# Kernel optimization log

Measured on AMD Instinct MI355X. Metric: run time of the kernel, lower is better.

Reference implementation:

```python
import jax, jax.numpy as jnp
import numpy as np

EPS = 1e-6
LAMB = 0.1
ITERS = 3


def setup_inputs() -> dict:
    key = jax.random.key(0)
    k = jax.random.split(key, 6)
    bi, bt, R, W, D = 128, 128, 36, 50, 1024
    return {
        "img_cls": jax.random.normal(k[0], (bi, D), jnp.float32),
        "imgs": jax.random.normal(k[1], (bi, R, D), jnp.float32),
        "cap_cls": jax.random.normal(k[2], (bt, D), jnp.float32),
        "caps": jax.random.normal(k[3], (bt, W, D), jnp.float32),
        "img_lens": jax.random.randint(k[4], (bi,), 1, R + 1, jnp.int32),
        "cap_lens": jax.random.randint(k[5], (bt,), 1, W + 1, jnp.int32),
    }


def _bregman(cost, mask, r, c):
    # P = exp(-cost/lamb) (masked entries have cost=+inf -> P=0), then
    # iterative row/col rescaling toward marginals r, c.
    P = jnp.where(mask, jnp.exp(-cost / LAMB), 0.0)
    P = P / (jnp.sum(P, axis=(-2, -1), keepdims=True) + EPS)
    for _ in range(ITERS):
        u = P.sum(axis=-1) + EPS          # [bi,bt,R]
        P = P * (r / u)[..., None]
        v = P.sum(axis=-2) + EPS          # [bi,bt,W]
        P = P * (c / v)[:, :, None, :]
    return P


def reference(img_cls, imgs, cap_cls, caps, img_lens, cap_lens):
    imgs = imgs + EPS
    caps = caps + EPS
    # prepend cls token
    imgs = jnp.concatenate([img_cls[:, None, :], imgs], axis=1)   # [bi,R+1,D]
    caps = jnp.concatenate([cap_cls[:, None, :], caps], axis=1)   # [bt,W+1,D]
    imgs = imgs / jnp.linalg.norm(imgs, axis=-1, keepdims=True)
    caps = caps / jnp.linalg.norm(caps, axis=-1, keepdims=True)
    # fine-grained cosine sims: [bi, bt, R+1, W+1]
    fg_sims = jnp.einsum("ird,twd->itrw", imgs, caps)
    il = img_lens + 1
    cl = cap_lens + 1
    R1, W1 = imgs.shape[1], caps.shape[1]
    rmask = jnp.arange(R1)[None, :] < il[:, None]   # [bi,R+1]
    wmask = jnp.arange(W1)[None, :] < cl[:, None]   # [bt,W+1]
    mask = rmask[:, None, :, None] & wmask[None, :, None, :]  # [bi,bt,R+1,W+1]
    # _ave_init: uniform marginals over valid rows/cols
    rvalid = mask.any(axis=-1).astype(fg_sims.dtype)  # [bi,bt,R+1]
    cvalid = mask.any(axis=-2).astype(fg_sims.dtype)  # [bi,bt,W+1]
    r = rvalid / rvalid.sum(axis=-1, keepdims=True)
    c = cvalid / cvalid.sum(axis=-1, keepdims=True)
    cost = 1.0 - fg_sims
    tp = _bregman(cost, mask, r, c)
    sims = jnp.sum(fg_sims * tp * mask.astype(fg_sims.dtype), axis=(-2, -1))
    return sims  # [bi, bt]
```

## Files before the change

### kernel.cpp

```cpp
#include <hip/hip_runtime.h>
#include <hip/hip_fp16.h>

#define EPSF 1e-6f

typedef _Float16 f16x8 __attribute__((ext_vector_type(8)));
typedef float f32x4 __attribute__((ext_vector_type(4)));

#define BK 64
#define SMEM_BYTES 37888
#define BUF_BYTES 10240

#define AS1 __attribute__((address_space(1)))
#define AS3 __attribute__((address_space(3)))

#define VM_WAIT(N) asm volatile("s_waitcnt vmcnt(" #N ")" ::: "memory")
#define LGKM0()    asm volatile("s_waitcnt lgkmcnt(0)" ::: "memory")

__device__ __forceinline__ float wave_sum_fast(float x) {
    asm volatile(
        "s_nop 1\n\t"
        "v_add_f32 %0, %0, %0 quad_perm:[1,0,3,2] row_mask:0xf bank_mask:0xf bound_ctrl:0\n\t"
        "s_nop 1\n\t"
        "v_add_f32 %0, %0, %0 quad_perm:[2,3,0,1] row_mask:0xf bank_mask:0xf bound_ctrl:0\n\t"
        "s_nop 1\n\t"
        "v_add_f32 %0, %0, %0 row_half_mirror row_mask:0xf bank_mask:0xf bound_ctrl:0\n\t"
        "s_nop 1\n\t"
        "v_add_f32 %0, %0, %0 row_mirror row_mask:0xf bank_mask:0xf bound_ctrl:0\n\t"
        "s_nop 1\n\t"
        "v_add_f32 %0, %0, %0 row_bcast:15 row_mask:0xf bank_mask:0xf bound_ctrl:0\n\t"
        "s_nop 1\n\t"
        "v_add_f32 %0, %0, %0 row_bcast:31 row_mask:0xf bank_mask:0xf bound_ctrl:0"
        : "+v"(x));
    return __int_as_float(__builtin_amdgcn_readlane(__float_as_int(x), 63));
}

__global__ __launch_bounds__(256) void norm_kernel(
        const float* __restrict__ img_cls, const float* __restrict__ imgs,
        const float* __restrict__ cap_cls, const float* __restrict__ caps,
        __half* __restrict__ Ah, __half* __restrict__ Bh) {
    __shared__ float red[4];
    const int row = blockIdx.x;
    const int tid = threadIdx.x;

    const float* src = nullptr;
    __half* dsth;
    float eps_add = EPSF;
    if (row < 64 * 80) {
        const int g = row / 80, r = row % 80;
        dsth = Ah + (size_t)row * 1024 + tid * 4;
        int i = -1, rr = 0;
        if (r < 37)      { i = 2 * g;     rr = r; }
        else if (r < 74) { i = 2 * g + 1; rr = r - 37; }
        if (i >= 0) {
            if (rr == 0) { src = img_cls + (size_t)i * 1024; eps_add = 0.0f; }
            else         { src = imgs + ((size_t)i * 36 + (rr - 1)) * 1024; }
        }
    } else {
        const int row2 = row - 64 * 80;
        const int t = row2 >> 6, r = row2 & 63;
        const int n = r >> 4, fr = r & 15;
        const int kt = tid >> 3, q4 = (tid >> 1) & 3, j = (tid & 1) * 4;
        dsth = Bh + ((size_t)(t * 32 + kt) * 4 + n) * 512 + (q4 * 16 + fr) * 8 + j;
        if (r == 0)       { src = cap_cls + (size_t)t * 1024; eps_add = 0.0f; }
        else if (r <= 50) { src = caps + ((size_t)t * 50 + (r - 1)) * 1024; }
    }

    if (src == nullptr) {
        ushort4 z; z.x = z.y = z.z = z.w = 0;
        *reinterpret_cast<ushort4*>(dsth) = z;
        return;
    }

    float4 v = reinterpret_cast<const float4*>(src)[tid];
    v.x += eps_add; v.y += eps_add; v.z += eps_add; v.w += eps_add;
    float ss = v.x * v.x + v.y * v.y + v.z * v.z + v.w * v.w;
    #pragma unroll
    for (int m = 1; m <= 32; m <<= 1) ss += __shfl_xor(ss, m);
    if ((tid & 63) == 0) red[tid >> 6] = ss;
    __syncthreads();
    const float tot = red[0] + red[1] + red[2] + red[3];
    const float rn = 1.0f / sqrtf(tot);

    ushort4 o;
    o.x = __half_as_ushort(__float2half(v.x * rn));
    o.y = __half_as_ushort(__float2half(v.y * rn));
    o.z = __half_as_ushort(__float2half(v.z * rn));
    o.w = __half_as_ushort(__float2half(v.w * rn));
    *reinterpret_cast<ushort4*>(dsth) = o;
}

__device__ __forceinline__ void stage_octA(const __half* __restrict__ Ag,
                                           __half* buf, int kb, int o, size_t lofs) {
    const __half* src = Ag + (size_t)o * 8192 + kb + lofs;
    __builtin_amdgcn_global_load_lds((const AS1 void*)src,
                                     (AS3 void*)(buf + o * 512), 16, 0, 0);
}

__device__ __forceinline__ void stage_A(const __half* __restrict__ Ag,
                                        __half* buf, int kb, int wave, size_t lofs) {
    stage_octA(Ag, buf, kb, wave, lofs);
    stage_octA(Ag, buf, kb, wave + 4, lofs);
    if (wave < 2) stage_octA(Ag, buf, kb, wave + 8, lofs);
}

template <int KS>
__device__ __forceinline__ void ds_af(const __half* buf, int fr, int q4,
                                      f16x8 af[5]) {
    const int soff = (((KS * 4 + q4) ^ (fr & 7)) * 8);
    #pragma unroll
    for (int m = 0; m < 5; ++m) {
        const int R = m * 16 + fr;
        af[m] = *reinterpret_cast<const f16x8*>(buf + R * BK + soff);
    }
}

__device__ __forceinline__ void load_bf2(const __half* __restrict__ Bgw, int k32,
                                         f16x8 bf[2]) {
    const __half* p = Bgw + (size_t)k32 * 2048;
    bf[0] = *reinterpret_cast<const f16x8*>(p);
    bf[1] = *reinterpret_cast<const f16x8*>(p + 512);
}

__device__ __forceinline__ void mfma_cluster(f32x4 acc[5][2], const f16x8 af[5],
                                             const f16x8 bf[2]) {
    __builtin_amdgcn_s_setprio(1);
    #pragma unroll
    for (int m = 0; m < 5; ++m)
        #pragma unroll
        for (int n = 0; n < 2; ++n)
            acc[m][n] = __builtin_amdgcn_mfma_f32_16x16x32_f16(af[m], bf[n], acc[m][n], 0, 0, 0);
    __builtin_amdgcn_s_setprio(0);
}

__global__ __launch_bounds__(256, 4) void fused_kernel(
        const __half* __restrict__ Ah, const __half* __restrict__ Bh,
        const int* __restrict__ img_lens, const int* __restrict__ cap_lens,
        float* __restrict__ out) {
    __shared__ __align__(16) char smem[SMEM_BYTES];
    __half* lds0 = reinterpret_cast<__half*>(smem);
    __half* lds1 = reinterpret_cast<__half*>(smem + BUF_BYTES);
    __half* lds2 = reinterpret_cast<__half*>(smem + 2 * BUF_BYTES);

    const int idx = blockIdx.x;
    const int xcd = idx & 7;
    const int within = idx >> 3;
    const int bx = within >> 3;
    const int by = xcd * 8 + (within & 7);

    const int tid = threadIdx.x;
    const int wave = tid >> 6;
    const int lane = tid & 63;
    const int fr = lane & 15;
    const int q4 = lane >> 4;

    const __half* Ag = Ah + (size_t)bx * 80 * 1024;
    const __half* Bgw = Bh + (size_t)(2 * by + (wave >> 1)) * 65536
                           + (size_t)((wave & 1) * 2) * 512 + lane * 8;

    const int rsub8 = lane >> 3;
    const int segsrc = (lane & 7) ^ rsub8;
    const size_t lofs = (size_t)rsub8 * 1024 + (size_t)(segsrc * 8);

    f32x4 acc[5][2];
    #pragma unroll
    for (int m = 0; m < 5; ++m)
        #pragma unroll
        for (int n = 0; n < 2; ++n) {
            f32x4 z = {0.0f, 0.0f, 0.0f, 0.0f};
            acc[m][n] = z;
        }

    f16x8 b0[2], b1[2], b2[2];

    load_bf2(Bgw, 0, b0);
    load_bf2(Bgw, 1, b1);
    stage_A(Ag, lds0, 0, wave, lofs);
    load_bf2(Bgw, 2, b2);
    stage_A(Ag, lds1, BK, wave, lofs);
    if (wave < 2) { VM_WAIT(5); } else { VM_WAIT(4); }
    __builtin_amdgcn_s_barrier();

    #define GEMM_TILE(KT, RD, ST, P0, P1, P2)                         \
    {                                                                 \
        f16x8 af[5];                                                  \
        ds_af<0>((RD), fr, q4, af);                                   \
        mfma_cluster(acc, af, (P0));                                  \
        load_bf2(Bgw, 2 * (KT) + 3, (P0));                            \
        ds_af<1>((RD), fr, q4, af);                                   \
        mfma_cluster(acc, af, (P1));                                  \
        load_bf2(Bgw, 2 * (KT) + 4, (P1));                            \
        LGKM0();                                                      \
        stage_A(Ag, (ST), ((KT) + 2) * BK, wave, lofs);               \
        if (wave < 2) { VM_WAIT(5); } else { VM_WAIT(4); }            \
        __builtin_amdgcn_s_barrier();                                 \
    }

    #pragma unroll 1
    for (int kt = 0; kt < 12; kt += 3) {
        GEMM_TILE(kt,     lds0, lds2, b0, b1, b2);
        GEMM_TILE(kt + 1, lds1, lds0, b2, b0, b1);
        GEMM_TILE(kt + 2, lds2, lds1, b1, b2, b0);
    }
    GEMM_TILE(12, lds0, lds2, b0, b1, b2);
    GEMM_TILE(13, lds1, lds0, b2, b0, b1);
    #undef GEMM_TILE

    {
        f16x8 af[5];
        ds_af<0>(lds2, fr, q4, af);
        mfma_cluster(acc, af, b1);
        load_bf2(Bgw, 31, b1);
        ds_af<1>(lds2, fr, q4, af);
        mfma_cluster(acc, af, b2);
        LGKM0();
        VM_WAIT(0);
        __builtin_amdgcn_s_barrier();
    }
    {
        f16x8 af[5];
        ds_af<0>(lds0, fr, q4, af);
        mfma_cluster(acc, af, b0);
        ds_af<1>(lds0, fr, q4, af);
        mfma_cluster(acc, af, b1);
    }

    __syncthreads();

    float* fgall = reinterpret_cast<float*>(smem);
    {
        const int ttw = wave >> 1;
        #pragma unroll
        for (int m = 0; m < 5; ++m) {
            #pragma unroll
            for (int q = 0; q < 4; ++q) {
                const int Rl = m * 16 + q4 * 4 + q;
                const int s = (Rl >= 37) ? 1 : 0;
                const int sr = Rl - 37 * s;
                const bool valid = (Rl < 74);
                const int rg = s * 2 + ttw;
                const int sw = ((sr >> 2) & 3) << 4;
                #pragma unroll
                for (int n = 0; n < 2; ++n) {
                    const int sc = (wave & 1) * 32 + n * 16 + fr;
                    if (valid)
                        fgall[rg * 2368 + sr * 64 + (sc ^ sw)] = acc[m][n][q];
                }
            }
        }
    }
    __syncthreads();

    {
        float* fg = fgall + wave * 2368;
        const int i = 2 * bx + (wave >> 1);
        const int t = 2 * by + (wave & 1);
        const int il = img_lens[i] + 1;
        const int cl = cap_lens[t] + 1;
        const bool vcol = lane < cl;

        #define FGR(r_) fg[(r_) * 64 + (lane ^ ((((r_) >> 2) & 3) << 4))]
        #define CEND(c_) ((((c_) * 8 + 8) < 37) ? ((c_) * 8 + 8) : 37)

        float P[37];
        #pragma unroll
        for (int r = 0; r < 37; ++r) P[r] = 0.0f;

        float ts[4] = {0.f, 0.f, 0.f, 0.f};
        #pragma unroll
        for (int c = 0; c < 5; ++c) {
            if (c * 8 < il) {
                #pragma unroll
                for (int r = c * 8; r < CEND(c); ++r) {
                    const float f = FGR(r);
                    const bool act = (r < il) && vcol;
                    const float pe = act ? __expf((f - 1.0f) * 10.0f) : 0.0f;
                    P[r] = pe;
                    ts[r & 3] += pe;
                }
            }
        }
        float tot = (ts[0] + ts[1]) + (ts[2] + ts[3]);
        tot = wave_sum_fast(tot);
        const float s0 = __builtin_amdgcn_rcpf(tot + EPSF);
        #pragma unroll
        for (int c = 0; c < 5; ++c) {
            if (c * 8 < il) {
                #pragma unroll
                for (int r = c * 8; r < CEND(c); ++r) P[r] *= s0;
            }
        }

        const float rmarg = 1.0f / (float)il;
        const float cmarg = 1.0f / (float)cl;
        float csave = 0.0f;
        for (int it = 0; it < 3; ++it) {
            #pragma unroll
            for (int c = 0; c < 5; ++c) {
                if (c * 8 < il) {
                    #pragma unroll
                    for (int r = c * 8; r < CEND(c); ++r) {
                        const float u = wave_sum_fast(P[r]);
                        P[r] *= rmarg * __builtin_amdgcn_rcpf(u + EPSF);
                    }
                }
            }
            float vs[4] = {EPSF, 0.f, 0.f, 0.f};
            #pragma unroll
            for (int c = 0; c < 5; ++c) {
                if (c * 8 < il) {
                    #pragma unroll
                    for (int r = c * 8; r < CEND(c); ++r) vs[r & 3] += P[r];
                }
            }
            const float v = (vs[0] + vs[1]) + (vs[2] + vs[3]);
            const float cs = vcol ? cmarg * __builtin_amdgcn_rcpf(v) : 0.0f;
            if (it < 2) {
                #pragma unroll
                for (int c = 0; c < 5; ++c) {
                    if (c * 8 < il) {
                        #pragma unroll
                        for (int r = c * 8; r < CEND(c); ++r) P[r] *= cs;
                    }
                }
            } else {
                csave = cs;
            }
        }

        float ls[4] = {0.f, 0.f, 0.f, 0.f};
        #pragma unroll
        for (int c = 0; c < 5; ++c) {
            if (c * 8 < il) {
                #pragma unroll
                for (int r = c * 8; r < CEND(c); ++r) {
                    const float f = FGR(r);
                    const float fm = (r < il) ? f : 0.0f;
                    ls[r & 3] = fmaf(fm, P[r], ls[r & 3]);
                }
            }
        }
        float local = csave * ((ls[0] + ls[1]) + (ls[2] + ls[3]));
        local = wave_sum_fast(local);
        if (lane == 0) out[i * 128 + t] = local;
        #undef FGR
        #undef CEND
    }
}

extern "C" void kernel_launch(void* const* d_in, const int* in_sizes, int n_in,
                              void* d_out, int out_size, void* d_ws, size_t ws_size,
                              hipStream_t stream) {
    const float* img_cls  = (const float*)d_in[0];
    const float* imgs     = (const float*)d_in[1];
    const float* cap_cls  = (const float*)d_in[2];
    const float* caps     = (const float*)d_in[3];
    const int*   img_lens = (const int*)d_in[4];
    const int*   cap_lens = (const int*)d_in[5];
    float* out = (float*)d_out;

    __half* Ah = (__half*)d_ws;
    __half* Bh = Ah + (size_t)64 * 80 * 1024;

    norm_kernel<<<64 * 80 + 128 * 64, 256, 0, stream>>>(img_cls, imgs, cap_cls, caps, Ah, Bh);
    fused_kernel<<<4096, 256, 0, stream>>>(Ah, Bh, img_lens, cap_lens, out);
}
```

Baseline: 140.9 us.

## Use four LDS buffers and process two K-tiles per barrier in GEMM

```diff
diff --git a/kernel.cpp b/kernel.cpp
--- a/kernel.cpp
+++ b/kernel.cpp
@@ -7,7 +7,7 @@
 typedef float f32x4 __attribute__((ext_vector_type(4)));
 
 #define BK 64
-#define SMEM_BYTES 37888
+#define SMEM_BYTES 40960
 #define BUF_BYTES 10240
 
 #define AS1 __attribute__((address_space(1)))
@@ -140,6 +140,7 @@
     __half* lds0 = reinterpret_cast<__half*>(smem);
     __half* lds1 = reinterpret_cast<__half*>(smem + BUF_BYTES);
     __half* lds2 = reinterpret_cast<__half*>(smem + 2 * BUF_BYTES);
+    __half* lds3 = reinterpret_cast<__half*>(smem + 3 * BUF_BYTES);
 
     const int idx = blockIdx.x;
     const int xcd = idx & 7;
@@ -175,35 +176,63 @@
     load_bf2(Bgw, 0, b0);
     load_bf2(Bgw, 1, b1);
     stage_A(Ag, lds0, 0, wave, lofs);
+    stage_A(Ag, lds1, BK, wave, lofs);
     load_bf2(Bgw, 2, b2);
-    stage_A(Ag, lds1, BK, wave, lofs);
-    if (wave < 2) { VM_WAIT(5); } else { VM_WAIT(4); }
+    stage_A(Ag, lds2, 2 * BK, wave, lofs);
+    stage_A(Ag, lds3, 3 * BK, wave, lofs);
+    if (wave < 2) { VM_WAIT(8); } else { VM_WAIT(6); }
     __builtin_amdgcn_s_barrier();
 
-    #define GEMM_TILE(KT, RD, ST, P0, P1, P2)                         \
+    {
+        f16x8 af[5];
+        ds_af<0>(lds0, fr, q4, af);
+        mfma_cluster(acc, af, b0);
+        load_bf2(Bgw, 3, b0);
+        ds_af<1>(lds0, fr, q4, af);
+        mfma_cluster(acc, af, b1);
+        load_bf2(Bgw, 4, b1);
+        VM_WAIT(2);
+        ds_af<0>(lds1, fr, q4, af);
+        mfma_cluster(acc, af, b2);
+        load_bf2(Bgw, 5, b2);
+        ds_af<1>(lds1, fr, q4, af);
+        mfma_cluster(acc, af, b0);
+        load_bf2(Bgw, 6, b0);
+        LGKM0();
+        VM_WAIT(2);
+        __builtin_amdgcn_s_barrier();
+    }
+
+    #define SSTEP(T, R0, R1, S0, S1, X, Y, Z)                         \
     {                                                                 \
         f16x8 af[5];                                                  \
-        ds_af<0>((RD), fr, q4, af);                                   \
-        mfma_cluster(acc, af, (P0));                                  \
-        load_bf2(Bgw, 2 * (KT) + 3, (P0));                            \
-        ds_af<1>((RD), fr, q4, af);                                   \
-        mfma_cluster(acc, af, (P1));                                  \
-        load_bf2(Bgw, 2 * (KT) + 4, (P1));                            \
+        ds_af<0>((R0), fr, q4, af);                                   \
+        mfma_cluster(acc, af, (X));                                   \
+        load_bf2(Bgw, 2 * (T) + 3, (X));                              \
+        ds_af<1>((R0), fr, q4, af);                                   \
+        mfma_cluster(acc, af, (Y));                                   \
+        load_bf2(Bgw, 2 * (T) + 4, (Y));                              \
+        stage_A(Ag, (S0), ((T) + 2) * BK, wave, lofs);                \
+        stage_A(Ag, (S1), ((T) + 3) * BK, wave, lofs);                \
+        if (wave < 2) { VM_WAIT(8); } else { VM_WAIT(6); }            \
+        ds_af<0>((R1), fr, q4, af);                                   \
+        mfma_cluster(acc, af, (Z));                                   \
+        load_bf2(Bgw, 2 * (T) + 5, (Z));                              \
+        ds_af<1>((R1), fr, q4, af);                                   \
+        mfma_cluster(acc, af, (X));                                   \
+        load_bf2(Bgw, 2 * (T) + 6, (X));                              \
         LGKM0();                                                      \
-        stage_A(Ag, (ST), ((KT) + 2) * BK, wave, lofs);               \
-        if (wave < 2) { VM_WAIT(5); } else { VM_WAIT(4); }            \
+        VM_WAIT(2);                                                   \
         __builtin_amdgcn_s_barrier();                                 \
     }
 
-    #pragma unroll 1
-    for (int kt = 0; kt < 12; kt += 3) {
-        GEMM_TILE(kt,     lds0, lds2, b0, b1, b2);
-        GEMM_TILE(kt + 1, lds1, lds0, b2, b0, b1);
-        GEMM_TILE(kt + 2, lds2, lds1, b1, b2, b0);
-    }
-    GEMM_TILE(12, lds0, lds2, b0, b1, b2);
-    GEMM_TILE(13, lds1, lds0, b2, b0, b1);
-    #undef GEMM_TILE
+    SSTEP(2,  lds2, lds3, lds0, lds1, b1, b2, b0);
+    SSTEP(4,  lds0, lds1, lds2, lds3, b2, b0, b1);
+    SSTEP(6,  lds2, lds3, lds0, lds1, b0, b1, b2);
+    SSTEP(8,  lds0, lds1, lds2, lds3, b1, b2, b0);
+    SSTEP(10, lds2, lds3, lds0, lds1, b2, b0, b1);
+    SSTEP(12, lds0, lds1, lds2, lds3, b0, b1, b2);
+    #undef SSTEP
 
     {
         f16x8 af[5];
@@ -212,15 +241,10 @@
         load_bf2(Bgw, 31, b1);
         ds_af<1>(lds2, fr, q4, af);
         mfma_cluster(acc, af, b2);
-        LGKM0();
         VM_WAIT(0);
-        __builtin_amdgcn_s_barrier();
-    }
-    {
-        f16x8 af[5];
-        ds_af<0>(lds0, fr, q4, af);
+        ds_af<0>(lds3, fr, q4, af);
         mfma_cluster(acc, af, b0);
-        ds_af<1>(lds0, fr, q4, af);
+        ds_af<1>(lds3, fr, q4, af);
         mfma_cluster(acc, af, b1);
     }
 
```

New measurement: 138.9 us. About the same (-1.4%).
